# Performance work log

Measured on AMD Instinct MI355X. Metric: run time of the kernel, lower is better.

## Reference

```python
import jax, jax.numpy as jnp
import numpy as np

N, E, IN_DIM, HID, L, H = 50000, 1600000, 32, 128, 3, 4
O = HID // H  # 32 per-head out_feats
PI = 3.141592653589793


def _glorot(key, shape):
    fan_in, fan_out = shape[-2], shape[-1]
    s = jnp.sqrt(6.0 / (fan_in + fan_out))
    return jax.random.uniform(key, shape, jnp.float32, -s, s)


def setup_inputs() -> dict:
    key = jax.random.key(0)
    ks = jax.random.split(key, 32)
    inp = {
        'node_feats': jax.random.normal(ks[0], (N, IN_DIM), jnp.float32),
        'src': jax.random.randint(ks[1], (E,), 0, N, jnp.int32),
        'dst': jax.random.randint(ks[2], (E,), 0, N, jnp.int32),
        # input projection
        'W_in': _glorot(ks[3], (IN_DIM, HID)), 'b_in': jnp.zeros((HID,), jnp.float32),
        # per-layer GATv2 params, stacked over L layers
        'W_src': _glorot(ks[4], (L, HID, HID)), 'b_src': jnp.zeros((L, HID), jnp.float32),
        'W_dst': _glorot(ks[5], (L, HID, HID)), 'b_dst': jnp.zeros((L, HID), jnp.float32),
        'attn': _glorot(ks[6], (L, H, O)),
        'ln_g': jnp.ones((L, HID), jnp.float32), 'ln_b': jnp.zeros((L, HID), jnp.float32),
        # node MLP + heads
        'W1': _glorot(ks[7], (HID, HID)), 'b1': jnp.zeros((HID,), jnp.float32),
        'W2': _glorot(ks[8], (HID, HID)), 'b2': jnp.zeros((HID,), jnp.float32),
        'Wa': _glorot(ks[9], (HID, 2)), 'ba': jnp.zeros((2,), jnp.float32),
        'Wg': _glorot(ks[10], (HID, 1)), 'bg': jnp.zeros((1,), jnp.float32),
        'Wal': _glorot(ks[11], (HID, 1)), 'bal': jnp.zeros((1,), jnp.float32),
        'Wn': _glorot(ks[12], (HID, 1)), 'bn': jnp.zeros((1,), jnp.float32),
        'Wt': _glorot(ks[13], (HID, 1)), 'bt': jnp.zeros((1,), jnp.float32),
    }
    return inp


def _segment_softmax(scores, seg, n):
    m = jax.ops.segment_max(scores, seg, num_segments=n)
    m = jnp.where(jnp.isfinite(m), m, 0.0)
    e = jnp.exp(scores - m[seg])
    s = jax.ops.segment_sum(e, seg, num_segments=n)
    return e / (s[seg] + 1e-9)


def _gatv2_layer(h, src, dst, Ws, bs, Wd, bd, a, g, b):
    n = h.shape[0]
    hs = (h @ Ws + bs).reshape(n, H, O)   # feat_src [N,H,O]
    hd = (h @ Wd + bd).reshape(n, H, O)   # feat_dst [N,H,O]
    e = jax.nn.leaky_relu(hs[src] + hd[dst], 0.2)     # [E,H,O]
    sc = jnp.einsum('eho,ho->eh', e, a)               # attention scores
    al = _segment_softmax(sc, dst, n)                 # softmax over in-edges
    rst = jax.ops.segment_sum(al[:, :, None] * hs[src], dst, num_segments=n)
    rst = rst + h.reshape(n, H, O)        # GATv2 residual (identity res_fc)
    h_new = rst.reshape(n, HID)
    x = h + h_new                         # encoder residual (dropout=eval)
    mu = jnp.mean(x, -1, keepdims=True)
    var = jnp.var(x, -1, keepdims=True)
    x = (x - mu) / jnp.sqrt(var + 1e-5) * g + b       # LayerNorm
    return jax.nn.relu(x)


def _forward(node_feats, src, dst, W_in, b_in, W_src, b_src, W_dst, b_dst, attn,
             ln_g, ln_b, W1, b1, W2, b2, Wa, ba, Wg, bg, Wal, bal, Wn, bn, Wt, bt):
    n = node_feats.shape[0]
    loops = jnp.arange(n, dtype=src.dtype)            # dgl.add_self_loop
    s = jnp.concatenate([src, loops])
    d = jnp.concatenate([dst, loops])
    h = node_feats @ W_in + b_in
    for l in range(L):
        h = _gatv2_layer(h, s, d, W_src[l], b_src[l], W_dst[l], b_dst[l],
                         attn[l], ln_g[l], ln_b[l])
    graph_emb = jnp.mean(h, axis=0, keepdims=True)    # dgl.mean_nodes, batch=1
    node_emb = h
    z = jax.nn.relu(jax.nn.relu(node_emb @ W1 + b1) @ W2 + b2)
    action_logits = z @ Wa + ba
    gamma = 5.0 * jax.nn.sigmoid((z @ Wg + bg)[:, 0])
    alpha = 2.0 * jax.nn.sigmoid((z @ Wal + bal)[:, 0])
    noise = 1.0 * jax.nn.sigmoid((z @ Wn + bn)[:, 0])
    theta = jnp.tanh((z @ Wt + bt)[:, 0]) * PI
    spawn_params = jnp.stack([gamma, alpha, noise, theta], axis=-1)
    return graph_emb, node_emb, action_logits, spawn_params


def reference(node_feats, src, dst, W_in, b_in, W_src, b_src, W_dst, b_dst, attn,
              ln_g, ln_b, W1, b1, W2, b2, Wa, ba, Wg, bg, Wal, bal, Wn, bn, Wt, bt):
    return _forward(node_feats, src, dst, W_in, b_in, W_src, b_src, W_dst, b_dst,
                    attn, ln_g, ln_b, W1, b1, W2, b2, Wa, ba, Wg, bg, Wal, bal,
                    Wn, bn, Wt, bt)
```

## Files before the change

### kernel.cpp

```cpp
#include <hip/hip_runtime.h>
#include <hip/hip_bf16.h>

#define HID 128
#define NHEAD 4
#define CAP 96

typedef __attribute__((ext_vector_type(8))) short bf16x8;
typedef __attribute__((ext_vector_type(4))) float f32x4;
typedef __attribute__((ext_vector_type(2))) float f32x2;

#define TILE2 1024
__global__ __launch_bounds__(256) void partition_edges(
    const int* __restrict__ src, const int* __restrict__ dst,
    int* __restrict__ tails, uint2* __restrict__ buckets,
    int BCAP, int E, int qg) {
    __shared__ int warr[4][8];
    __shared__ int base_sh[8];
    const int tid = threadIdx.x;
    const int wave = tid >> 6, lane = tid & 63;
    const int e0 = blockIdx.x * TILE2;
    const unsigned long long below = (1ULL << lane) - 1ULL;

    int sreg[4], dreg[4], binr[4], rankr[4];
    int wcnt[8] = {0, 0, 0, 0, 0, 0, 0, 0};
#pragma unroll
    for (int j = 0; j < 4; ++j) {
        int idx = e0 + j * 256 + tid;
        bool ok = idx < E;
        int d = ok ? dst[idx] : 0;
        int s = ok ? src[idx] : 0;
        int g = ok ? (d / qg) : -1;
        sreg[j] = s; dreg[j] = d; binr[j] = g;
        int r = 0;
#pragma unroll
        for (int b = 0; b < 8; ++b) {
            unsigned long long mb = __ballot(g == b);
            if (g == b) r = wcnt[b] + (int)__popcll(mb & below);
            wcnt[b] += (int)__popcll(mb);
        }
        rankr[j] = r;
    }
    if (lane == 0) {
#pragma unroll
        for (int b = 0; b < 8; ++b) warr[wave][b] = wcnt[b];
    }
    __syncthreads();
    if (tid < 8) {
        int b = tid, tot = 0;
        int pre[4];
#pragma unroll
        for (int w = 0; w < 4; ++w) { pre[w] = tot; tot += warr[w][b]; }
        base_sh[b] = atomicAdd(&tails[b], tot);
#pragma unroll
        for (int w = 0; w < 4; ++w) warr[w][b] = pre[w];
    }
    __syncthreads();
#pragma unroll
    for (int j = 0; j < 4; ++j) {
        int g = binr[j];
        if (g >= 0) {
            int pos = base_sh[g] + warr[wave][g] + rankr[j];
            if (pos < BCAP)
                buckets[(size_t)g * BCAP + pos] = make_uint2((unsigned)sreg[j], (unsigned)dreg[j]);
        }
    }
}

__global__ __launch_bounds__(256) void fill_slots(
    const uint2* __restrict__ buckets, const int* __restrict__ tails,
    int* __restrict__ cnt, int* __restrict__ slots, int BCAP) {
    int g = blockIdx.x & 7;
    int blk = blockIdx.x >> 3;
    int nblk = gridDim.x >> 3;
    int c = tails[g]; if (c > BCAP) c = BCAP;
    const uint2* b = buckets + (size_t)g * BCAP;
    for (int i = blk * 256 + threadIdx.x; i < c; i += nblk * 256) {
        uint2 e = b[i];
        int pos = atomicAdd(&cnt[e.y], 1);
        if (pos < CAP) slots[(size_t)e.y * CAP + pos] = (int)e.x;
    }
}

__device__ __forceinline__ unsigned pack2_bf16_rne(float lo, float hi) {
    unsigned a = __float_as_uint(lo);
    a = (a + 0x7fffu + ((a >> 16) & 1u)) >> 16;
    unsigned b = __float_as_uint(hi);
    b = (b + 0x7fffu + ((b >> 16) & 1u)) & 0xffff0000u;
    return a | b;
}

__device__ __forceinline__ unsigned short bf16_rne(float x) {
    unsigned u = __float_as_uint(x);
    u = (u + 0x7fffu + ((u >> 16) & 1u)) >> 16;
    return (unsigned short)u;
}

__device__ __forceinline__ f32x2 unpack_bf(unsigned u) {
    f32x2 r;
    r.x = __uint_as_float(u << 16);
    r.y = __uint_as_float(u & 0xffff0000u);
    return r;
}

__device__ __forceinline__ f32x2 leaky2(f32x2 q) {
    return __builtin_elementwise_max(q, q * 0.2f);
}

__device__ __forceinline__ float row_sum4(float x) {
    x += __int_as_float(__builtin_amdgcn_update_dpp(0, __float_as_int(x), 0xB1, 0xF, 0xF, true));
    x += __int_as_float(__builtin_amdgcn_update_dpp(0, __float_as_int(x), 0x4E, 0xF, 0xF, true));
    return x;
}

__global__ void prep_weights(const float* __restrict__ W_src, const float* __restrict__ W_dst,
                             const float* __restrict__ W1, const float* __restrict__ W2,
                             unsigned short* __restrict__ Wt) {
    int mat = blockIdx.x;
    const float* Wf = (mat < 3) ? (W_src + (size_t)mat * 16384)
                    : (mat < 6) ? (W_dst + (size_t)(mat - 3) * 16384)
                    : (mat == 6) ? W1 : W2;
    unsigned short* out = Wt + (size_t)mat * 16384;
    for (int idx = threadIdx.x; idx < 16384; idx += blockDim.x) {
        int k = idx >> 7, nn = idx & 127;
        out[nn * 128 + k] = bf16_rne(Wf[idx]);
    }
}

#define GR 64
template <int K, bool RELU, bool F32OUT, bool BF16OUT>
__global__ __launch_bounds__(256) void gemm_k(const float* __restrict__ A,
                                              const float* __restrict__ W,
                                              const float* __restrict__ bias,
                                              float* __restrict__ Cf,
                                              unsigned short* __restrict__ C16, int n) {
    __shared__ __align__(16) float a_sh[GR * K];
    const int tid = threadIdx.x;
    const int tx = tid & 31;
    const int ty = tid >> 5;
    const int r0 = blockIdx.x * GR;

    for (int i = tid * 4; i < GR * K; i += 1024) {
        int r = i / K, k = i % K;
        int gr = r0 + r;
        float4 v = make_float4(0.f, 0.f, 0.f, 0.f);
        if (gr < n) v = *(const float4*)&A[(size_t)gr * K + k];
        *(float4*)&a_sh[i] = v;
    }
    __syncthreads();

    float4 acc[8];
#pragma unroll
    for (int r = 0; r < 8; ++r) acc[r] = make_float4(0.f, 0.f, 0.f, 0.f);

    const float* ab = &a_sh[ty * 8 * K];
    const float* wb = &W[tx * 4];

    for (int k = 0; k < K; k += 4) {
        float4 w0 = *(const float4*)&wb[(size_t)(k + 0) * 128];
        float4 w1 = *(const float4*)&wb[(size_t)(k + 1) * 128];
        float4 w2 = *(const float4*)&wb[(size_t)(k + 2) * 128];
        float4 w3 = *(const float4*)&wb[(size_t)(k + 3) * 128];
#pragma unroll
        for (int r = 0; r < 8; ++r) {
            float4 a4 = *(const float4*)&ab[r * K + k];
            acc[r].x = fmaf(a4.x, w0.x, acc[r].x);
            acc[r].y = fmaf(a4.x, w0.y, acc[r].y);
            acc[r].z = fmaf(a4.x, w0.z, acc[r].z);
            acc[r].w = fmaf(a4.x, w0.w, acc[r].w);
            acc[r].x = fmaf(a4.y, w1.x, acc[r].x);
            acc[r].y = fmaf(a4.y, w1.y, acc[r].y);
            acc[r].z = fmaf(a4.y, w1.z, acc[r].z);
            acc[r].w = fmaf(a4.y, w1.w, acc[r].w);
            acc[r].x = fmaf(a4.z, w2.x, acc[r].x);
            acc[r].y = fmaf(a4.z, w2.y, acc[r].y);
            acc[r].z = fmaf(a4.z, w2.z, acc[r].z);
            acc[r].w = fmaf(a4.z, w2.w, acc[r].w);
            acc[r].x = fmaf(a4.w, w3.x, acc[r].x);
            acc[r].y = fmaf(a4.w, w3.y, acc[r].y);
            acc[r].z = fmaf(a4.w, w3.z, acc[r].z);
            acc[r].w = fmaf(a4.w, w3.w, acc[r].w);
        }
    }

    float4 b4 = *(const float4*)&bias[tx * 4];
#pragma unroll
    for (int r = 0; r < 8; ++r) {
        int gr = r0 + ty * 8 + r;
        if (gr < n) {
            float4 o;
            o.x = acc[r].x + b4.x;
            o.y = acc[r].y + b4.y;
            o.z = acc[r].z + b4.z;
            o.w = acc[r].w + b4.w;
            if (RELU) {
                o.x = fmaxf(o.x, 0.f); o.y = fmaxf(o.y, 0.f);
                o.z = fmaxf(o.z, 0.f); o.w = fmaxf(o.w, 0.f);
            }
            if (F32OUT) *(float4*)&Cf[(size_t)gr * 128 + tx * 4] = o;
            if (BF16OUT) {
                uint2 st;
                st.x = pack2_bf16_rne(o.x, o.y);
                st.y = pack2_bf16_rne(o.z, o.w);
                *(uint2*)&C16[(size_t)gr * 128 + tx * 4] = st;
            }
        }
    }
}

template <bool RELU, bool F32OUT, bool BF16OUT>
__global__ __launch_bounds__(256) void gemm_mfma(
    const unsigned short* __restrict__ A16,
    const unsigned short* __restrict__ Bt16,
    const float* __restrict__ bias,
    float* __restrict__ Cf, unsigned short* __restrict__ C16, int n) {
    const int wave = threadIdx.x >> 6;
    const int lane = threadIdx.x & 63;
    const int r = lane & 15, g = lane >> 4;
    const int m0 = blockIdx.x * 64 + wave * 16;
    int ra = m0 + r; if (ra > n - 1) ra = n - 1;
    const bf16x8* Arow = (const bf16x8*)(A16 + (size_t)ra * 128);
    bf16x8 a0 = Arow[g];
    bf16x8 a1 = Arow[4 + g];
    bf16x8 a2 = Arow[8 + g];
    bf16x8 a3 = Arow[12 + g];
    const int row = m0 + r;
    const bool rok = row < n;
#pragma unroll
    for (int ct = 0; ct < 8; ++ct) {
        const bf16x8* Brow = (const bf16x8*)(Bt16 + (size_t)(ct * 16 + r) * 128);
        f32x4 acc = {0.f, 0.f, 0.f, 0.f};
        acc = __builtin_amdgcn_mfma_f32_16x16x32_bf16(Brow[g], a0, acc, 0, 0, 0);
        acc = __builtin_amdgcn_mfma_f32_16x16x32_bf16(Brow[4 + g], a1, acc, 0, 0, 0);
        acc = __builtin_amdgcn_mfma_f32_16x16x32_bf16(Brow[8 + g], a2, acc, 0, 0, 0);
        acc = __builtin_amdgcn_mfma_f32_16x16x32_bf16(Brow[12 + g], a3, acc, 0, 0, 0);
        const int col = ct * 16 + g * 4;
        float4 b4 = *(const float4*)&bias[col];
        float o0 = acc[0] + b4.x, o1 = acc[1] + b4.y;
        float o2 = acc[2] + b4.z, o3 = acc[3] + b4.w;
        if (RELU) {
            o0 = fmaxf(o0, 0.f); o1 = fmaxf(o1, 0.f);
            o2 = fmaxf(o2, 0.f); o3 = fmaxf(o3, 0.f);
        }
        if (rok) {
            if (F32OUT)
                *(float4*)&Cf[(size_t)row * 128 + col] = make_float4(o0, o1, o2, o3);
            if (BF16OUT) {
                uint2 st;
                st.x = pack2_bf16_rne(o0, o1);
                st.y = pack2_bf16_rne(o2, o3);
                *(uint2*)&C16[(size_t)row * 128 + col] = st;
            }
        }
    }
}

__global__ __launch_bounds__(256) void gemm_mfma_dual(
    const unsigned short* __restrict__ A16,
    const unsigned short* __restrict__ B1t, const unsigned short* __restrict__ B2t,
    const float* __restrict__ bias1, const float* __restrict__ bias2,
    unsigned short* __restrict__ C1, unsigned short* __restrict__ C2, int n) {
    const int wave = threadIdx.x >> 6;
    const int lane = threadIdx.x & 63;
    const int r = lane & 15, g = lane >> 4;
    const int m0 = blockIdx.x * 64 + wave * 16;
    int ra = m0 + r; if (ra > n - 1) ra = n - 1;
    const bf16x8* Arow = (const bf16x8*)(A16 + (size_t)ra * 128);
    bf16x8 a0 = Arow[g];
    bf16x8 a1 = Arow[4 + g];
    bf16x8 a2 = Arow[8 + g];
    bf16x8 a3 = Arow[12 + g];
    const int row = m0 + r;
    const bool rok = row < n;
#pragma unroll
    for (int ct = 0; ct < 8; ++ct) {
        const int col = ct * 16 + g * 4;
        {
            const bf16x8* Brow = (const bf16x8*)(B1t + (size_t)(ct * 16 + r) * 128);
            f32x4 acc = {0.f, 0.f, 0.f, 0.f};
            acc = __builtin_amdgcn_mfma_f32_16x16x32_bf16(Brow[g], a0, acc, 0, 0, 0);
            acc = __builtin_amdgcn_mfma_f32_16x16x32_bf16(Brow[4 + g], a1, acc, 0, 0, 0);
            acc = __builtin_amdgcn_mfma_f32_16x16x32_bf16(Brow[8 + g], a2, acc, 0, 0, 0);
            acc = __builtin_amdgcn_mfma_f32_16x16x32_bf16(Brow[12 + g], a3, acc, 0, 0, 0);
            float4 b4 = *(const float4*)&bias1[col];
            if (rok) {
                uint2 st;
                st.x = pack2_bf16_rne(acc[0] + b4.x, acc[1] + b4.y);
                st.y = pack2_bf16_rne(acc[2] + b4.z, acc[3] + b4.w);
                *(uint2*)&C1[(size_t)row * 128 + col] = st;
            }
        }
        {
            const bf16x8* Brow = (const bf16x8*)(B2t + (size_t)(ct * 16 + r) * 128);
            f32x4 acc = {0.f, 0.f, 0.f, 0.f};
            acc = __builtin_amdgcn_mfma_f32_16x16x32_bf16(Brow[g], a0, acc, 0, 0, 0);
            acc = __builtin_amdgcn_mfma_f32_16x16x32_bf16(Brow[4 + g], a1, acc, 0, 0, 0);
            acc = __builtin_amdgcn_mfma_f32_16x16x32_bf16(Brow[8 + g], a2, acc, 0, 0, 0);
            acc = __builtin_amdgcn_mfma_f32_16x16x32_bf16(Brow[12 + g], a3, acc, 0, 0, 0);
            float4 b4 = *(const float4*)&bias2[col];
            if (rok) {
                uint2 st;
                st.x = pack2_bf16_rne(acc[0] + b4.x, acc[1] + b4.y);
                st.y = pack2_bf16_rne(acc[2] + b4.z, acc[3] + b4.w);
                *(uint2*)&C2[(size_t)row * 128 + col] = st;
            }
        }
    }
}

__global__ __launch_bounds__(256) void gat_aggregate(
    const float* __restrict__ h,
    const unsigned short* __restrict__ hs16,
    const unsigned short* __restrict__ hd16,
    const int* __restrict__ cnt,
    const int* __restrict__ slots,
    const float* __restrict__ attn,
    const float* __restrict__ ln_g, const float* __restrict__ ln_b,
    float* __restrict__ h_out, unsigned* __restrict__ h16_out, int n) {
    int v = (blockIdx.x * blockDim.x + threadIdx.x) >> 6;
    int lane = threadIdx.x & 63;
    if (v >= n) return;
    const int lh = lane & 15;
    const int quarter = lane >> 4;
    const int f0 = lh * 8;
    const unsigned fb = (unsigned)lh << 4;

    const float L2E = 1.4426950408889634f;
    f32x2 av0, av1, av2, av3;
    {
        float4 aa = *(const float4*)&attn[f0];
        float4 ab = *(const float4*)&attn[f0 + 4];
        av0 = (f32x2){aa.x, aa.y} * L2E; av1 = (f32x2){aa.z, aa.w} * L2E;
        av2 = (f32x2){ab.x, ab.y} * L2E; av3 = (f32x2){ab.z, ab.w} * L2E;
    }
    const char* hsb = (const char*)hs16;
    f32x2 hd0, hd1, hd2, hd3;
    {
        uint4 wd = *(const uint4*)((const char*)hd16 + ((size_t)(unsigned)v << 8) + fb);
        hd0 = unpack_bf(wd.x); hd1 = unpack_bf(wd.y);
        hd2 = unpack_bf(wd.z); hd3 = unpack_bf(wd.w);
    }
    uint4 wv = *(const uint4*)(hsb + ((size_t)(unsigned)v << 8) + fb);
    f32x2 sv0 = unpack_bf(wv.x), sv1 = unpack_bf(wv.y);
    f32x2 sv2 = unpack_bf(wv.z), sv3 = unpack_bf(wv.w);
    float m;
    {
        f32x2 q0 = leaky2(sv0 + hd0), q1 = leaky2(sv1 + hd1);
        f32x2 q2 = leaky2(sv2 + hd2), q3 = leaky2(sv3 + hd3);
        f32x2 dt = q0 * av0; dt += q1 * av1; dt += q2 * av2; dt += q3 * av3;
        m = row_sum4(dt.x + dt.y);
    }
    const bool q0lane = (quarter == 0);
    float s = q0lane ? 1.f : 0.f;
    f32x2 acc0 = q0lane ? sv0 : (f32x2){0.f, 0.f};
    f32x2 acc1 = q0lane ? sv1 : (f32x2){0.f, 0.f};
    f32x2 acc2 = q0lane ? sv2 : (f32x2){0.f, 0.f};
    f32x2 acc3 = q0lane ? sv3 : (f32x2){0.f, 0.f};

    int deg = cnt[v]; if (deg > CAP) deg = CAP;
    const int* srow = slots + (size_t)v * CAP;
    int end4 = deg & ~3;

    auto process = [&](uint4 w) {
        f32x2 g0 = unpack_bf(w.x), g1 = unpack_bf(w.y);
        f32x2 g2 = unpack_bf(w.z), g3 = unpack_bf(w.w);
        f32x2 p0 = leaky2(g0 + hd0), p1 = leaky2(g1 + hd1);
        f32x2 p2 = leaky2(g2 + hd2), p3 = leaky2(g3 + hd3);
        f32x2 dt = p0 * av0; dt += p1 * av1; dt += p2 * av2; dt += p3 * av3;
        float sc = row_sum4(dt.x + dt.y);
        float d0 = sc - m;
        if (__builtin_expect(__any(d0 > 8.f), 0)) {
            float dmx = fmaxf(d0, __shfl_xor(d0, 16));
            dmx = fmaxf(dmx, __shfl_xor(dmx, 32));
            float mn = m + fmaxf(dmx, 0.f);
            float rr = exp2f(m - mn);
            s *= rr; acc0 *= rr; acc1 *= rr; acc2 *= rr; acc3 *= rr;
            m = mn; d0 = sc - m;
        }
        float e = exp2f(d0);
        s += e;
        acc0 += g0 * e; acc1 += g1 * e; acc2 += g2 * e; acc3 += g3 * e;
    };

    if (end4 > 0) {
        uint4 w = *(const uint4*)(hsb + ((size_t)(unsigned)srow[quarter] << 8) + fb);
        int un = (4 < end4) ? srow[4 + quarter] : 0;
        for (int i = 4; i < end4; i += 4) {
            uint4 wn = *(const uint4*)(hsb + ((size_t)(unsigned)un << 8) + fb);
            if (i + 4 < end4) un = srow[i + 4 + quarter];
            process(w);
            w = wn;
        }
        process(w);
    }
    if (end4 < deg) {
        int idx = end4 + quarter;
        bool act = idx < deg;
        int u = srow[act ? idx : end4];
        uint4 w = *(const uint4*)(hsb + ((size_t)(unsigned)u << 8) + fb);
        f32x2 g0 = unpack_bf(w.x), g1 = unpack_bf(w.y);
        f32x2 g2 = unpack_bf(w.z), g3 = unpack_bf(w.w);
        f32x2 p0 = leaky2(g0 + hd0), p1 = leaky2(g1 + hd1);
        f32x2 p2 = leaky2(g2 + hd2), p3 = leaky2(g3 + hd3);
        f32x2 dt = p0 * av0; dt += p1 * av1; dt += p2 * av2; dt += p3 * av3;
        float sc = row_sum4(dt.x + dt.y);
        float d0 = sc - m;
        float d0m = act ? d0 : -1e30f;
        if (__builtin_expect(__any(d0m > 8.f), 0)) {
            float dmx = fmaxf(d0m, __shfl_xor(d0m, 16));
            dmx = fmaxf(dmx, __shfl_xor(dmx, 32));
            float mn = m + fmaxf(dmx, 0.f);
            float rr = exp2f(m - mn);
            s *= rr; acc0 *= rr; acc1 *= rr; acc2 *= rr; acc3 *= rr;
            m = mn; d0 = sc - m;
        }
        float e = act ? exp2f(d0) : 0.f;
        s += e;
        acc0 += g0 * e; acc1 += g1 * e; acc2 += g2 * e; acc3 += g3 * e;
    }
#pragma unroll
    for (int d = 16; d <= 32; d <<= 1) {
        s += __shfl_xor(s, d);
        acc0.x += __shfl_xor(acc0.x, d); acc0.y += __shfl_xor(acc0.y, d);
        acc1.x += __shfl_xor(acc1.x, d); acc1.y += __shfl_xor(acc1.y, d);
        acc2.x += __shfl_xor(acc2.x, d); acc2.y += __shfl_xor(acc2.y, d);
        acc3.x += __shfl_xor(acc3.x, d); acc3.y += __shfl_xor(acc3.y, d);
    }
    float inv = 1.0f / (s + 1e-9f);

    f32x2 hv0, hv1, hv2, hv3;
    {
        float4 ha = *(const float4*)&h[(size_t)v * 128 + f0];
        float4 hb = *(const float4*)&h[(size_t)v * 128 + f0 + 4];
        hv0 = (f32x2){ha.x, ha.y}; hv1 = (f32x2){ha.z, ha.w};
        hv2 = (f32x2){hb.x, hb.y}; hv3 = (f32x2){hb.z, hb.w};
    }
    f32x2 x0 = acc0 * inv + hv0 * 2.f;
    f32x2 x1 = acc1 * inv + hv1 * 2.f;
    f32x2 x2 = acc2 * inv + hv2 * 2.f;
    f32x2 x3 = acc3 * inv + hv3 * 2.f;

    f32x2 sum2 = (x0 + x1) + (x2 + x3);
    f32x2 sq2 = x0 * x0 + x1 * x1 + x2 * x2 + x3 * x3;
    float sum = sum2.x + sum2.y, sq = sq2.x + sq2.y;
#pragma unroll
    for (int d = 1; d < 64; d <<= 1) { sum += __shfl_xor(sum, d); sq += __shfl_xor(sq, d); }
    float mu = sum * (1.f / 512.f);
    float var = sq * (1.f / 512.f) - mu * mu;
    float rstd = rsqrtf(var + 1e-5f);
    f32x2 g0v, g1v, g2v, g3v, b0v, b1v, b2v, b3v;
    {
        float4 ga = *(const float4*)&ln_g[f0];
        float4 gb = *(const float4*)&ln_g[f0 + 4];
        float4 ba = *(const float4*)&ln_b[f0];
        float4 bb = *(const float4*)&ln_b[f0 + 4];
        g0v = (f32x2){ga.x, ga.y}; g1v = (f32x2){ga.z, ga.w};
        g2v = (f32x2){gb.x, gb.y}; g3v = (f32x2){gb.z, gb.w};
        b0v = (f32x2){ba.x, ba.y}; b1v = (f32x2){ba.z, ba.w};
        b2v = (f32x2){bb.x, bb.y}; b3v = (f32x2){bb.z, bb.w};
    }
    f32x2 zero = {0.f, 0.f};
    f32x2 y0 = __builtin_elementwise_max((x0 - mu) * rstd * g0v + b0v, zero);
    f32x2 y1 = __builtin_elementwise_max((x1 - mu) * rstd * g1v + b1v, zero);
    f32x2 y2 = __builtin_elementwise_max((x2 - mu) * rstd * g2v + b2v, zero);
    f32x2 y3 = __builtin_elementwise_max((x3 - mu) * rstd * g3v + b3v, zero);
    if (quarter == 0) {
        float* orow = &h_out[(size_t)v * 128 + f0];
        *(float4*)orow = make_float4(y0.x, y0.y, y1.x, y1.y);
        *(float4*)(orow + 4) = make_float4(y2.x, y2.y, y3.x, y3.y);
        uint4 st;
        st.x = pack2_bf16_rne(y0.x, y0.y);
        st.y = pack2_bf16_rne(y1.x, y1.y);
        st.z = pack2_bf16_rne(y2.x, y2.y);
        st.w = pack2_bf16_rne(y3.x, y3.y);
        *(uint4*)((char*)h16_out + ((size_t)v << 8) + fb) = st;
    }
}

__global__ __launch_bounds__(256) void mean_partial(const float4* __restrict__ src,
                                                    float* __restrict__ gacc, size_t n4) {
    int tid = threadIdx.x;
    size_t i = blockIdx.x * (size_t)256 + tid;
    size_t stride = (size_t)gridDim.x * 256;
    float ax = 0.f, ay = 0.f, az = 0.f, aw = 0.f;
    for (; i < n4; i += stride) {
        float4 v = src[i];
        ax += v.x; ay += v.y; az += v.z; aw += v.w;
    }
    __shared__ float4 sb[256];
    sb[tid] = make_float4(ax, ay, az, aw);
    __syncthreads();
    for (int off = 128; off >= 32; off >>= 1) {
        if (tid < off) {
            float4 o = sb[tid + off];
            sb[tid].x += o.x; sb[tid].y += o.y; sb[tid].z += o.z; sb[tid].w += o.w;
        }
        __syncthreads();
    }
    if (tid < 32) {
        float4 a = sb[tid];
        atomicAdd(&gacc[tid * 4 + 0], a.x);
        atomicAdd(&gacc[tid * 4 + 1], a.y);
        atomicAdd(&gacc[tid * 4 + 2], a.z);
        atomicAdd(&gacc[tid * 4 + 3], a.w);
    }
}

__global__ void graph_mean_final(const float* __restrict__ gacc, float* __restrict__ out, int n) {
    int c = threadIdx.x;
    out[c] = gacc[c] / (float)n;
}

__global__ __launch_bounds__(256) void heads_kernel(
    const float* __restrict__ z,
    const float* __restrict__ Wa, const float* __restrict__ ba,
    const float* __restrict__ Wg, const float* __restrict__ bg,
    const float* __restrict__ Wal, const float* __restrict__ bal,
    const float* __restrict__ Wn, const float* __restrict__ bn,
    const float* __restrict__ Wt, const float* __restrict__ bt,
    float* __restrict__ logits, float* __restrict__ spawn, int n) {
    int v = (blockIdx.x * blockDim.x + threadIdx.x) >> 6;
    int lane = threadIdx.x & 63;
    if (v >= n) return;
    int f0 = lane * 2;
    float2 zv = *(const float2*)&z[(size_t)v * 128 + f0];
    float p0 = zv.x * Wa[f0 * 2]     + zv.y * Wa[(f0 + 1) * 2];
    float p1 = zv.x * Wa[f0 * 2 + 1] + zv.y * Wa[(f0 + 1) * 2 + 1];
    float p2 = zv.x * Wg[f0]  + zv.y * Wg[f0 + 1];
    float p3 = zv.x * Wal[f0] + zv.y * Wal[f0 + 1];
    float p4 = zv.x * Wn[f0]  + zv.y * Wn[f0 + 1];
    float p5 = zv.x * Wt[f0]  + zv.y * Wt[f0 + 1];
#pragma unroll
    for (int d = 1; d < 64; d <<= 1) {
        p0 += __shfl_xor(p0, d); p1 += __shfl_xor(p1, d); p2 += __shfl_xor(p2, d);
        p3 += __shfl_xor(p3, d); p4 += __shfl_xor(p4, d); p5 += __shfl_xor(p5, d);
    }
    if (lane == 0) {
        logits[(size_t)v * 2 + 0] = p0 + ba[0];
        logits[(size_t)v * 2 + 1] = p1 + ba[1];
        float gamma = 5.f / (1.f + __expf(-(p2 + bg[0])));
        float alpha = 2.f / (1.f + __expf(-(p3 + bal[0])));
        float noise = 1.f / (1.f + __expf(-(p4 + bn[0])));
        float theta = tanhf(p5 + bt[0]) * 3.14159265358979323846f;
        spawn[(size_t)v * 4 + 0] = gamma;
        spawn[(size_t)v * 4 + 1] = alpha;
        spawn[(size_t)v * 4 + 2] = noise;
        spawn[(size_t)v * 4 + 3] = theta;
    }
}

extern "C" void kernel_launch(void* const* d_in, const int* in_sizes, int n_in,
                              void* d_out, int out_size, void* d_ws, size_t ws_size,
                              hipStream_t stream) {
    const float* node_feats = (const float*)d_in[0];
    const int*   src  = (const int*)d_in[1];
    const int*   dst  = (const int*)d_in[2];
    const float* W_in = (const float*)d_in[3];
    const float* b_in = (const float*)d_in[4];
    const float* W_src = (const float*)d_in[5];
    const float* b_src = (const float*)d_in[6];
    const float* W_dst = (const float*)d_in[7];
    const float* b_dst = (const float*)d_in[8];
    const float* attn  = (const float*)d_in[9];
    const float* ln_g  = (const float*)d_in[10];
    const float* ln_b  = (const float*)d_in[11];
    const float* W1 = (const float*)d_in[12]; const float* b1 = (const float*)d_in[13];
    const float* W2 = (const float*)d_in[14]; const float* b2 = (const float*)d_in[15];
    const float* Wa = (const float*)d_in[16]; const float* ba = (const float*)d_in[17];
    const float* Wg = (const float*)d_in[18]; const float* bg = (const float*)d_in[19];
    const float* Wal = (const float*)d_in[20]; const float* bal = (const float*)d_in[21];
    const float* Wn = (const float*)d_in[22]; const float* bn = (const float*)d_in[23];
    const float* Wt = (const float*)d_in[24]; const float* bt = (const float*)d_in[25];

    const int n = in_sizes[0] / 32;
    const int E = in_sizes[1];
    const int qg = (n + 7) / 8;
    const int BCAP = 240 * 1024;
    const int ntiles = (E + TILE2 - 1) / TILE2;

    char* ws = (char*)d_ws;
    size_t off = 0;
    auto alloc = [&](size_t bytes) -> void* {
        void* p = ws + off;
        off = (off + bytes + 255) & ~(size_t)255;
        return p;
    };
    float* Bh0 = (float*)alloc((size_t)n * 128 * 4);
    float* Bh1 = (float*)alloc((size_t)n * 128 * 4);
    float* Bz  = (float*)alloc((size_t)n * 128 * 4);
    unsigned short* h16  = (unsigned short*)alloc((size_t)n * 128 * 2);
    unsigned short* hs16 = (unsigned short*)alloc((size_t)n * 128 * 2);
    unsigned short* hd16 = (unsigned short*)alloc((size_t)n * 128 * 2);
    unsigned short* Wt16 = (unsigned short*)alloc((size_t)8 * 16384 * 2);
    int* cnt   = (int*)alloc((size_t)n * 4);
    int* slots = (int*)alloc((size_t)n * CAP * 4);
    uint2* buckets = (uint2*)alloc((size_t)8 * BCAP * 8);
    int* tails = (int*)alloc(8 * 4);
    float* gacc = (float*)alloc(128 * 4);

    float* out = (float*)d_out;
    float* out_gemb   = out;
    float* out_nemb   = out + 128;
    float* out_logits = out + 128 + (size_t)n * 128;
    float* out_spawn  = out_logits + (size_t)n * 2;

    hipMemsetAsync(cnt, 0, (size_t)n * 4, stream);
    hipMemsetAsync(tails, 0, 8 * 4, stream);
    hipMemsetAsync(gacc, 0, 128 * 4, stream);

    partition_edges<<<ntiles, 256, 0, stream>>>(src, dst, tails, buckets, BCAP, E, qg);
    fill_slots<<<2048, 256, 0, stream>>>(buckets, tails, cnt, slots, BCAP);

    prep_weights<<<8, 256, 0, stream>>>(W_src, W_dst, W1, W2, Wt16);

    int gemm_grid = (n + GR - 1) / GR;
    int mfma_grid = (n + 63) / 64;

    gemm_k<32, false, true, true><<<gemm_grid, 256, 0, stream>>>(node_feats, W_in, b_in, Bh0, h16, n);

    float* cur = Bh0;
    for (int l = 0; l < 3; ++l) {
        gemm_mfma_dual<<<mfma_grid, 256, 0, stream>>>(
            h16, Wt16 + (size_t)l * 16384, Wt16 + (size_t)(3 + l) * 16384,
            b_src + l * 128, b_dst + l * 128, hs16, hd16, n);
        float* nxt = (l == 2) ? out_nemb : ((cur == Bh0) ? Bh1 : Bh0);
        gat_aggregate<<<(n + 3) / 4, 256, 0, stream>>>(cur, hs16, hd16, cnt, slots,
                                                       attn + l * 128, ln_g + l * 128,
                                                       ln_b + l * 128, nxt, (unsigned*)h16, n);
        cur = nxt;
    }

    gemm_mfma<true, false, true><<<mfma_grid, 256, 0, stream>>>(
        h16, Wt16 + (size_t)6 * 16384, b1, nullptr, hs16, n);
    gemm_mfma<true, true, false><<<mfma_grid, 256, 0, stream>>>(
        hs16, Wt16 + (size_t)7 * 16384, b2, Bz, nullptr, n);

    mean_partial<<<512, 256, 0, stream>>>((const float4*)out_nemb, gacc, (size_t)n * 32);
    graph_mean_final<<<1, 128, 0, stream>>>(gacc, out_gemb, n);
    heads_kernel<<<(n + 3) / 4, 256, 0, stream>>>(Bz, Wa, ba, Wg, bg, Wal, bal,
                                                  Wn, bn, Wt, bt, out_logits, out_spawn, n);
}
```

Measured before the change: 577.1 us.

## Pack edges to 32-bit, keep residual in bf16, fuse small kernels

```diff
diff --git a/kernel.cpp b/kernel.cpp
--- a/kernel.cpp
+++ b/kernel.cpp
@@ -9,11 +9,57 @@
 typedef __attribute__((ext_vector_type(4))) float f32x4;
 typedef __attribute__((ext_vector_type(2))) float f32x2;
 
+__device__ __forceinline__ unsigned pack2_bf16_rne(float lo, float hi) {
+    unsigned a = __float_as_uint(lo);
+    a = (a + 0x7fffu + ((a >> 16) & 1u)) >> 16;
+    unsigned b = __float_as_uint(hi);
+    b = (b + 0x7fffu + ((b >> 16) & 1u)) & 0xffff0000u;
+    return a | b;
+}
+
+__device__ __forceinline__ unsigned short bf16_rne(float x) {
+    unsigned u = __float_as_uint(x);
+    u = (u + 0x7fffu + ((u >> 16) & 1u)) >> 16;
+    return (unsigned short)u;
+}
+
+__device__ __forceinline__ f32x2 unpack_bf(unsigned u) {
+    f32x2 r;
+    r.x = __uint_as_float(u << 16);
+    r.y = __uint_as_float(u & 0xffff0000u);
+    return r;
+}
+
+__device__ __forceinline__ f32x2 leaky2(f32x2 q) {
+    return __builtin_elementwise_max(q, q * 0.2f);
+}
+
+__device__ __forceinline__ float row_sum4(float x) {
+    x += __int_as_float(__builtin_amdgcn_update_dpp(0, __float_as_int(x), 0xB1, 0xF, 0xF, true));
+    x += __int_as_float(__builtin_amdgcn_update_dpp(0, __float_as_int(x), 0x4E, 0xF, 0xF, true));
+    return x;
+}
+
 #define TILE2 1024
-__global__ __launch_bounds__(256) void partition_edges(
+__global__ __launch_bounds__(256) void partition_and_prep(
     const int* __restrict__ src, const int* __restrict__ dst,
-    int* __restrict__ tails, uint2* __restrict__ buckets,
-    int BCAP, int E, int qg) {
+    int* __restrict__ tails, unsigned* __restrict__ buckets,
+    int BCAP, int E, int qg, int ntiles,
+    const float* __restrict__ W_src, const float* __restrict__ W_dst,
+    const float* __restrict__ W1, const float* __restrict__ W2,
+    unsigned short* __restrict__ Wt) {
+    if ((int)blockIdx.x >= ntiles) {
+        int mat = blockIdx.x - ntiles;
+        const float* Wf = (mat < 3) ? (W_src + (size_t)mat * 16384)
+                        : (mat < 6) ? (W_dst + (size_t)(mat - 3) * 16384)
+                        : (mat == 6) ? W1 : W2;
+        unsigned short* out = Wt + (size_t)mat * 16384;
+        for (int idx = threadIdx.x; idx < 16384; idx += blockDim.x) {
+            int k = idx >> 7, nn = idx & 127;
+            out[nn * 128 + k] = bf16_rne(Wf[idx]);
+        }
+        return;
+    }
     __shared__ int warr[4][8];
     __shared__ int base_sh[8];
     const int tid = threadIdx.x;
@@ -21,7 +67,8 @@
     const int e0 = blockIdx.x * TILE2;
     const unsigned long long below = (1ULL << lane) - 1ULL;
 
-    int sreg[4], dreg[4], binr[4], rankr[4];
+    unsigned preg[4];
+    int binr[4], rankr[4];
     int wcnt[8] = {0, 0, 0, 0, 0, 0, 0, 0};
 #pragma unroll
     for (int j = 0; j < 4; ++j) {
@@ -30,7 +77,9 @@
         int d = ok ? dst[idx] : 0;
         int s = ok ? src[idx] : 0;
         int g = ok ? (d / qg) : -1;
-        sreg[j] = s; dreg[j] = d; binr[j] = g;
+        int dl = d - g * qg;
+        preg[j] = (unsigned)s | ((unsigned)dl << 16);
+        binr[j] = g;
         int r = 0;
 #pragma unroll
         for (int b = 0; b < 8; ++b) {
@@ -60,79 +109,34 @@
         int g = binr[j];
         if (g >= 0) {
             int pos = base_sh[g] + warr[wave][g] + rankr[j];
-            if (pos < BCAP)
-                buckets[(size_t)g * BCAP + pos] = make_uint2((unsigned)sreg[j], (unsigned)dreg[j]);
+            if (pos < BCAP) buckets[(size_t)g * BCAP + pos] = preg[j];
         }
     }
 }
 
 __global__ __launch_bounds__(256) void fill_slots(
-    const uint2* __restrict__ buckets, const int* __restrict__ tails,
-    int* __restrict__ cnt, int* __restrict__ slots, int BCAP) {
+    const unsigned* __restrict__ buckets, const int* __restrict__ tails,
+    int* __restrict__ cnt, int* __restrict__ slots, int BCAP, int qg) {
     int g = blockIdx.x & 7;
     int blk = blockIdx.x >> 3;
     int nblk = gridDim.x >> 3;
     int c = tails[g]; if (c > BCAP) c = BCAP;
-    const uint2* b = buckets + (size_t)g * BCAP;
+    int dbase = g * qg;
+    const unsigned* b = buckets + (size_t)g * BCAP;
     for (int i = blk * 256 + threadIdx.x; i < c; i += nblk * 256) {
-        uint2 e = b[i];
-        int pos = atomicAdd(&cnt[e.y], 1);
-        if (pos < CAP) slots[(size_t)e.y * CAP + pos] = (int)e.x;
-    }
-}
-
-__device__ __forceinline__ unsigned pack2_bf16_rne(float lo, float hi) {
-    unsigned a = __float_as_uint(lo);
-    a = (a + 0x7fffu + ((a >> 16) & 1u)) >> 16;
-    unsigned b = __float_as_uint(hi);
-    b = (b + 0x7fffu + ((b >> 16) & 1u)) & 0xffff0000u;
-    return a | b;
-}
-
-__device__ __forceinline__ unsigned short bf16_rne(float x) {
-    unsigned u = __float_as_uint(x);
-    u = (u + 0x7fffu + ((u >> 16) & 1u)) >> 16;
-    return (unsigned short)u;
-}
-
-__device__ __forceinline__ f32x2 unpack_bf(unsigned u) {
-    f32x2 r;
-    r.x = __uint_as_float(u << 16);
-    r.y = __uint_as_float(u & 0xffff0000u);
-    return r;
-}
-
-__device__ __forceinline__ f32x2 leaky2(f32x2 q) {
-    return __builtin_elementwise_max(q, q * 0.2f);
-}
-
-__device__ __forceinline__ float row_sum4(float x) {
-    x += __int_as_float(__builtin_amdgcn_update_dpp(0, __float_as_int(x), 0xB1, 0xF, 0xF, true));
-    x += __int_as_float(__builtin_amdgcn_update_dpp(0, __float_as_int(x), 0x4E, 0xF, 0xF, true));
-    return x;
-}
-
-__global__ void prep_weights(const float* __restrict__ W_src, const float* __restrict__ W_dst,
-                             const float* __restrict__ W1, const float* __restrict__ W2,
-                             unsigned short* __restrict__ Wt) {
-    int mat = blockIdx.x;
-    const float* Wf = (mat < 3) ? (W_src + (size_t)mat * 16384)
-                    : (mat < 6) ? (W_dst + (size_t)(mat - 3) * 16384)
-                    : (mat == 6) ? W1 : W2;
-    unsigned short* out = Wt + (size_t)mat * 16384;
-    for (int idx = threadIdx.x; idx < 16384; idx += blockDim.x) {
-        int k = idx >> 7, nn = idx & 127;
-        out[nn * 128 + k] = bf16_rne(Wf[idx]);
+        unsigned p = b[i];
+        int d = dbase + (int)(p >> 16);
+        int pos = atomicAdd(&cnt[d], 1);
+        if (pos < CAP) slots[(size_t)d * CAP + pos] = (int)(p & 0xFFFFu);
     }
 }
 
 #define GR 64
-template <int K, bool RELU, bool F32OUT, bool BF16OUT>
-__global__ __launch_bounds__(256) void gemm_k(const float* __restrict__ A,
-                                              const float* __restrict__ W,
-                                              const float* __restrict__ bias,
-                                              float* __restrict__ Cf,
-                                              unsigned short* __restrict__ C16, int n) {
+__global__ __launch_bounds__(256) void gemm_in(const float* __restrict__ A,
+                                               const float* __restrict__ W,
+                                               const float* __restrict__ bias,
+                                               unsigned short* __restrict__ C16, int n) {
+    const int K = 32;
     __shared__ __align__(16) float a_sh[GR * K];
     const int tid = threadIdx.x;
     const int tx = tid & 31;
@@ -187,22 +191,10 @@
     for (int r = 0; r < 8; ++r) {
         int gr = r0 + ty * 8 + r;
         if (gr < n) {
-            float4 o;
-            o.x = acc[r].x + b4.x;
-            o.y = acc[r].y + b4.y;
-            o.z = acc[r].z + b4.z;
-            o.w = acc[r].w + b4.w;
-            if (RELU) {
-                o.x = fmaxf(o.x, 0.f); o.y = fmaxf(o.y, 0.f);
-                o.z = fmaxf(o.z, 0.f); o.w = fmaxf(o.w, 0.f);
-            }
-            if (F32OUT) *(float4*)&Cf[(size_t)gr * 128 + tx * 4] = o;
-            if (BF16OUT) {
-                uint2 st;
-                st.x = pack2_bf16_rne(o.x, o.y);
-                st.y = pack2_bf16_rne(o.z, o.w);
-                *(uint2*)&C16[(size_t)gr * 128 + tx * 4] = st;
-            }
+            uint2 st;
+            st.x = pack2_bf16_rne(acc[r].x + b4.x, acc[r].y + b4.y);
+            st.y = pack2_bf16_rne(acc[r].z + b4.z, acc[r].w + b4.w);
+            *(uint2*)&C16[(size_t)gr * 128 + tx * 4] = st;
         }
     }
 }
@@ -307,15 +299,16 @@
     }
 }
 
+template <bool LAST>
 __global__ __launch_bounds__(256) void gat_aggregate(
-    const float* __restrict__ h,
+    unsigned short* __restrict__ h16,
     const unsigned short* __restrict__ hs16,
     const unsigned short* __restrict__ hd16,
     const int* __restrict__ cnt,
     const int* __restrict__ slots,
     const float* __restrict__ attn,
     const float* __restrict__ ln_g, const float* __restrict__ ln_b,
-    float* __restrict__ h_out, unsigned* __restrict__ h16_out, int n) {
+    float* __restrict__ out_f32, int n) {
     int v = (blockIdx.x * blockDim.x + threadIdx.x) >> 6;
     int lane = threadIdx.x & 63;
     if (v >= n) return;
@@ -429,10 +422,9 @@
 
     f32x2 hv0, hv1, hv2, hv3;
     {
-        float4 ha = *(const float4*)&h[(size_t)v * 128 + f0];
-        float4 hb = *(const float4*)&h[(size_t)v * 128 + f0 + 4];
-        hv0 = (f32x2){ha.x, ha.y}; hv1 = (f32x2){ha.z, ha.w};
-        hv2 = (f32x2){hb.x, hb.y}; hv3 = (f32x2){hb.z, hb.w};
+        uint4 wh = *(const uint4*)((const char*)h16 + ((size_t)(unsigned)v << 8) + fb);
+        hv0 = unpack_bf(wh.x); hv1 = unpack_bf(wh.y);
+        hv2 = unpack_bf(wh.z); hv3 = unpack_bf(wh.w);
     }
     f32x2 x0 = acc0 * inv + hv0 * 2.f;
     f32x2 x1 = acc1 * inv + hv1 * 2.f;
@@ -464,61 +456,60 @@
     f32x2 y2 = __builtin_elementwise_max((x2 - mu) * rstd * g2v + b2v, zero);
     f32x2 y3 = __builtin_elementwise_max((x3 - mu) * rstd * g3v + b3v, zero);
     if (quarter == 0) {
-        float* orow = &h_out[(size_t)v * 128 + f0];
-        *(float4*)orow = make_float4(y0.x, y0.y, y1.x, y1.y);
-        *(float4*)(orow + 4) = make_float4(y2.x, y2.y, y3.x, y3.y);
         uint4 st;
         st.x = pack2_bf16_rne(y0.x, y0.y);
         st.y = pack2_bf16_rne(y1.x, y1.y);
         st.z = pack2_bf16_rne(y2.x, y2.y);
         st.w = pack2_bf16_rne(y3.x, y3.y);
-        *(uint4*)((char*)h16_out + ((size_t)v << 8) + fb) = st;
-    }
-}
-
-__global__ __launch_bounds__(256) void mean_partial(const float4* __restrict__ src,
-                                                    float* __restrict__ gacc, size_t n4) {
-    int tid = threadIdx.x;
-    size_t i = blockIdx.x * (size_t)256 + tid;
-    size_t stride = (size_t)gridDim.x * 256;
-    float ax = 0.f, ay = 0.f, az = 0.f, aw = 0.f;
-    for (; i < n4; i += stride) {
-        float4 v = src[i];
-        ax += v.x; ay += v.y; az += v.z; aw += v.w;
-    }
-    __shared__ float4 sb[256];
-    sb[tid] = make_float4(ax, ay, az, aw);
-    __syncthreads();
-    for (int off = 128; off >= 32; off >>= 1) {
-        if (tid < off) {
-            float4 o = sb[tid + off];
-            sb[tid].x += o.x; sb[tid].y += o.y; sb[tid].z += o.z; sb[tid].w += o.w;
-        }
-        __syncthreads();
-    }
-    if (tid < 32) {
-        float4 a = sb[tid];
-        atomicAdd(&gacc[tid * 4 + 0], a.x);
-        atomicAdd(&gacc[tid * 4 + 1], a.y);
-        atomicAdd(&gacc[tid * 4 + 2], a.z);
-        atomicAdd(&gacc[tid * 4 + 3], a.w);
-    }
-}
-
-__global__ void graph_mean_final(const float* __restrict__ gacc, float* __restrict__ out, int n) {
-    int c = threadIdx.x;
-    out[c] = gacc[c] / (float)n;
-}
-
-__global__ __launch_bounds__(256) void heads_kernel(
+        *(uint4*)((char*)h16 + ((size_t)v << 8) + fb) = st;
+        if (LAST) {
+            float* orow = &out_f32[(size_t)v * 128 + f0];
+            *(float4*)orow = make_float4(y0.x, y0.y, y1.x, y1.y);
+            *(float4*)(orow + 4) = make_float4(y2.x, y2.y, y3.x, y3.y);
+        }
+    }
+}
+
+__global__ __launch_bounds__(256) void mean_and_heads(
+    const float* __restrict__ nemb, float* __restrict__ gacc,
     const float* __restrict__ z,
     const float* __restrict__ Wa, const float* __restrict__ ba,
     const float* __restrict__ Wg, const float* __restrict__ bg,
     const float* __restrict__ Wal, const float* __restrict__ bal,
     const float* __restrict__ Wn, const float* __restrict__ bn,
     const float* __restrict__ Wt, const float* __restrict__ bt,
-    float* __restrict__ logits, float* __restrict__ spawn, int n) {
-    int v = (blockIdx.x * blockDim.x + threadIdx.x) >> 6;
+    float* __restrict__ logits, float* __restrict__ spawn, int n, int MB) {
+    if ((int)blockIdx.x < MB) {
+        const float4* src = (const float4*)nemb;
+        size_t n4 = (size_t)n * 32;
+        int tid = threadIdx.x;
+        size_t i = blockIdx.x * (size_t)256 + tid;
+        size_t stride = (size_t)MB * 256;
+        float ax = 0.f, ay = 0.f, az = 0.f, aw = 0.f;
+        for (; i < n4; i += stride) {
+            float4 v = src[i];
+            ax += v.x; ay += v.y; az += v.z; aw += v.w;
+        }
+        __shared__ float4 sb[256];
+        sb[tid] = make_float4(ax, ay, az, aw);
+        __syncthreads();
+        for (int off = 128; off >= 32; off >>= 1) {
+            if (tid < off) {
+                float4 o = sb[tid + off];
+                sb[tid].x += o.x; sb[tid].y += o.y; sb[tid].z += o.z; sb[tid].w += o.w;
+            }
+            __syncthreads();
+        }
+        if (tid < 32) {
+            float4 a = sb[tid];
+            atomicAdd(&gacc[tid * 4 + 0], a.x);
+            atomicAdd(&gacc[tid * 4 + 1], a.y);
+            atomicAdd(&gacc[tid * 4 + 2], a.z);
+            atomicAdd(&gacc[tid * 4 + 3], a.w);
+        }
+        return;
+    }
+    int v = (((int)blockIdx.x - MB) * blockDim.x + (int)threadIdx.x) >> 6;
     int lane = threadIdx.x & 63;
     if (v >= n) return;
     int f0 = lane * 2;
@@ -546,6 +537,11 @@
         spawn[(size_t)v * 4 + 2] = noise;
         spawn[(size_t)v * 4 + 3] = theta;
     }
+}
+
+__global__ void graph_mean_final(const float* __restrict__ gacc, float* __restrict__ out, int n) {
+    int c = threadIdx.x;
+    out[c] = gacc[c] / (float)n;
 }
 
 extern "C" void kernel_launch(void* const* d_in, const int* in_sizes, int n_in,
@@ -584,8 +580,6 @@
         off = (off + bytes + 255) & ~(size_t)255;
         return p;
     };
-    float* Bh0 = (float*)alloc((size_t)n * 128 * 4);
-    float* Bh1 = (float*)alloc((size_t)n * 128 * 4);
     float* Bz  = (float*)alloc((size_t)n * 128 * 4);
     unsigned short* h16  = (unsigned short*)alloc((size_t)n * 128 * 2);
     unsigned short* hs16 = (unsigned short*)alloc((size_t)n * 128 * 2);
@@ -593,7 +587,7 @@
     unsigned short* Wt16 = (unsigned short*)alloc((size_t)8 * 16384 * 2);
     int* cnt   = (int*)alloc((size_t)n * 4);
     int* slots = (int*)alloc((size_t)n * CAP * 4);
-    uint2* buckets = (uint2*)alloc((size_t)8 * BCAP * 8);
+    unsigned* buckets = (unsigned*)alloc((size_t)8 * BCAP * 4);
     int* tails = (int*)alloc(8 * 4);
     float* gacc = (float*)alloc(128 * 4);
 
@@ -607,26 +601,27 @@
     hipMemsetAsync(tails, 0, 8 * 4, stream);
     hipMemsetAsync(gacc, 0, 128 * 4, stream);
 
-    partition_edges<<<ntiles, 256, 0, stream>>>(src, dst, tails, buckets, BCAP, E, qg);
-    fill_slots<<<2048, 256, 0, stream>>>(buckets, tails, cnt, slots, BCAP);
-
-    prep_weights<<<8, 256, 0, stream>>>(W_src, W_dst, W1, W2, Wt16);
+    partition_and_prep<<<ntiles + 8, 256, 0, stream>>>(
+        src, dst, tails, buckets, BCAP, E, qg, ntiles, W_src, W_dst, W1, W2, Wt16);
+    fill_slots<<<2048, 256, 0, stream>>>(buckets, tails, cnt, slots, BCAP, qg);
 
     int gemm_grid = (n + GR - 1) / GR;
     int mfma_grid = (n + 63) / 64;
 
-    gemm_k<32, false, true, true><<<gemm_grid, 256, 0, stream>>>(node_feats, W_in, b_in, Bh0, h16, n);
-
-    float* cur = Bh0;
+    gemm_in<<<gemm_grid, 256, 0, stream>>>(node_feats, W_in, b_in, h16, n);
+
     for (int l = 0; l < 3; ++l) {
         gemm_mfma_dual<<<mfma_grid, 256, 0, stream>>>(
             h16, Wt16 + (size_t)l * 16384, Wt16 + (size_t)(3 + l) * 16384,
             b_src + l * 128, b_dst + l * 128, hs16, hd16, n);
-        float* nxt = (l == 2) ? out_nemb : ((cur == Bh0) ? Bh1 : Bh0);
-        gat_aggregate<<<(n + 3) / 4, 256, 0, stream>>>(cur, hs16, hd16, cnt, slots,
-                                                       attn + l * 128, ln_g + l * 128,
-                                                       ln_b + l * 128, nxt, (unsigned*)h16, n);
-        cur = nxt;
+        if (l == 2)
+            gat_aggregate<true><<<(n + 3) / 4, 256, 0, stream>>>(
+                h16, hs16, hd16, cnt, slots, attn + l * 128, ln_g + l * 128,
+                ln_b + l * 128, out_nemb, n);
+        else
+            gat_aggregate<false><<<(n + 3) / 4, 256, 0, stream>>>(
+                h16, hs16, hd16, cnt, slots, attn + l * 128, ln_g + l * 128,
+                ln_b + l * 128, nullptr, n);
     }
 
     gemm_mfma<true, false, true><<<mfma_grid, 256, 0, stream>>>(
@@ -634,8 +629,9 @@
     gemm_mfma<true, true, false><<<mfma_grid, 256, 0, stream>>>(
         hs16, Wt16 + (size_t)7 * 16384, b2, Bz, nullptr, n);
 
-    mean_partial<<<512, 256, 0, stream>>>((const float4*)out_nemb, gacc, (size_t)n * 32);
+    const int MB = 512;
+    mean_and_heads<<<MB + (n + 3) / 4, 256, 0, stream>>>(
+        out_nemb, gacc, Bz, Wa, ba, Wg, bg, Wal, bal, Wn, bn, Wt, bt,
+        out_logits, out_spawn, n, MB);
     graph_mean_final<<<1, 128, 0, stream>>>(gacc, out_gemb, n);
-    heads_kernel<<<(n + 3) / 4, 256, 0, stream>>>(Bz, Wa, ba, Wg, bg, Wal, bal,
-                                                  Wn, bn, Wt, bt, out_logits, out_spawn, n);
-}
+}
```

After: 555.5 us. -3.8%, faster.
